# Performance work log

Measured on AMD Instinct MI355X. Metric: run time of the kernel, lower is better.

Reference implementation:

```python
import jax, jax.numpy as jnp
import numpy as np

N = 2_000_000  # total nodes across batch
F = 16         # eigenvector coefficient dim
B = 8          # number of graphs in batch (2^B sign combos)

def setup_inputs() -> dict:
    key = jax.random.key(0)
    k1, k2, k3 = jax.random.split(key, 3)
    inp = jax.random.normal(k1, (N, F), dtype=jnp.float32)
    tgt = jax.random.normal(k2, (N, F), dtype=jnp.float32)
    batch = jnp.sort(jax.random.randint(k3, (N,), 0, B, dtype=jnp.int32))
    return {"input": inp, "target": tgt, "batch": batch, "batch_size": B}

def reference(input, target, batch, batch_size):
    # loss(s) = sum((s_{batch} * x - t)^2) = sum(x^2) + sum(t^2) - 2 * sum_g s_g * dot_g
    # where dot_g = sum_{i in graph g} <x_i, t_i>.  Min over s in {+1,-1}^B is the
    # exact value produced by the original 2^B brute-force loop (reduction='sum').
    per_node = jnp.sum(input * target, axis=-1)                      # [N]
    dots = jax.ops.segment_sum(per_node, batch, num_segments=batch_size)  # [B]
    base = jnp.sum(input * input) + jnp.sum(target * target)         # scalar
    # enumerate all 2^B sign combinations (tiny, graph-level)
    idx = jnp.arange(2 ** batch_size)
    bits = (idx[:, None] >> jnp.arange(batch_size)[None, :]) & 1     # [2^B, B]
    signs = (1 - 2 * bits).astype(dots.dtype)                        # {+1,-1}
    losses = base - 2.0 * (signs @ dots)                             # [2^B]
    return jnp.min(losses)
```

## Files before the change

### kernel.cpp

```cpp
#include <hip/hip_runtime.h>

#define BLOCK 256
#define GRID  2048
#define NGRAPH 8
#define U 4
#define TILE (BLOCK * U)


__global__ __launch_bounds__(BLOCK) void reduce_kernel(
    const float4* __restrict__ x4,
    const float4* __restrict__ t4,
    const int*    __restrict__ batch,
    float* __restrict__ g_acc,
    int M )
{
    __shared__ float s_acc[NGRAPH + 1];
    const int tid = threadIdx.x;
    if (tid < NGRAPH + 1) s_acc[tid] = 0.0f;
    __syncthreads();

    float acc[NGRAPH];
    #pragma unroll
    for (int i = 0; i < NGRAPH; ++i) acc[i] = 0.0f;
    float base = 0.0f;

    const int nfull  = M / TILE;
    const int ntiles = (M + TILE - 1) / TILE;

    #define ACCUM(a, c, b)                                                 \
        do {                                                               \
            base += a.x*a.x + a.y*a.y + a.z*a.z + a.w*a.w                  \
                  + c.x*c.x + c.y*c.y + c.z*c.z + c.w*c.w;                 \
            const float d_ = a.x*c.x + a.y*c.y + a.z*c.z + a.w*c.w;        \
            _Pragma("unroll")                                              \
            for (int i = 0; i < NGRAPH; ++i)                               \
                acc[i] += (b == i) ? d_ : 0.0f;                            \
        } while (0)

    for (int t = blockIdx.x; t < ntiles; t += GRID) {
        const int e0 = t * TILE + tid;
        if (t < nfull) {
            const float4 a0 = x4[e0            ];
            const float4 a1 = x4[e0 +     BLOCK];
            const float4 a2 = x4[e0 + 2 * BLOCK];
            const float4 a3 = x4[e0 + 3 * BLOCK];
            const float4 c0 = t4[e0            ];
            const float4 c1 = t4[e0 +     BLOCK];
            const float4 c2 = t4[e0 + 2 * BLOCK];
            const float4 c3 = t4[e0 + 3 * BLOCK];
            const int    b0 = batch[(e0            ) >> 2];
            const int    b1 = batch[(e0 +     BLOCK) >> 2];
            const int    b2 = batch[(e0 + 2 * BLOCK) >> 2];
            const int    b3 = batch[(e0 + 3 * BLOCK) >> 2];

            ACCUM(a0, c0, b0);
            ACCUM(a1, c1, b1);
            ACCUM(a2, c2, b2);
            ACCUM(a3, c3, b3);
        } else {
            #pragma unroll
            for (int j = 0; j < U; ++j) {
                const int e = e0 + j * BLOCK;
                if (e < M) {
                    const float4 a = x4[e];
                    const float4 c = t4[e];
                    const int    b = batch[e >> 2];
                    ACCUM(a, c, b);
                }
            }
        }
    }
    #undef ACCUM

    #pragma unroll
    for (int i = 0; i <= NGRAPH; ++i) {
        float v = (i < NGRAPH) ? acc[i] : base;
        #pragma unroll
        for (int off = 32; off > 0; off >>= 1)
            v += __shfl_xor(v, off, 64);
        if ((tid & 63) == 0)
            atomicAdd(&s_acc[i], v);
    }
    __syncthreads();

    if (tid <= NGRAPH)
        atomicAdd(&g_acc[tid], s_acc[tid]);
}

__global__ void finalize_kernel(const float* __restrict__ g_acc,
                                float* __restrict__ out)
{
    if (threadIdx.x == 0) {
        float s = 0.0f;
        #pragma unroll
        for (int i = 0; i < NGRAPH; ++i) s += fabsf(g_acc[i]);
        out[0] = g_acc[NGRAPH] - 2.0f * s;
    }
}

extern "C" void kernel_launch(void* const* d_in, const int* in_sizes, int n_in,
                              void* d_out, int out_size, void* d_ws, size_t ws_size,
                              hipStream_t stream) {
    const float* inp   = (const float*)d_in[0];
    const float* tgt   = (const float*)d_in[1];
    const int*   batch = (const int*)d_in[2];

    const long long Nrows = (long long)in_sizes[0] / 16;
    const int       M     = (int)(Nrows * 4);

    float* g_acc = (float*)d_ws;
    hipMemsetAsync(g_acc, 0, (NGRAPH + 1) * sizeof(float), stream);

    reduce_kernel<<<GRID, BLOCK, 0, stream>>>(
        (const float4*)inp, (const float4*)tgt, batch, g_acc, M);

    finalize_kernel<<<1, 64, 0, stream>>>(g_acc, (float*)d_out);
}
```

Before: 276.3 us.

## Software-pipeline tile loads with double-buffered registers and sched barriers

Reorganizes the grid-stride loop into a two-stage software pipeline: the next tile's loads are issued into a second register set before the current tile is consumed, and sched_barrier calls stop the compiler from reordering them. The per-tile unroll drops from 4 to 2 so the two buffers keep register use similar, and the partial tail tile is handled once after the loop. The goal is to keep more memory requests in flight per wave on this bandwidth-bound reduction. In exchange, each tile carries fewer loads, and the fixed scheduling may block optimizations the compiler would otherwise make.

```diff
diff --git a/kernel.cpp b/kernel.cpp
--- a/kernel.cpp
+++ b/kernel.cpp
@@ -3,7 +3,7 @@
 #define BLOCK 256
 #define GRID  2048
 #define NGRAPH 8
-#define U 4
+#define U 2
 #define TILE (BLOCK * U)
 
 
@@ -24,8 +24,10 @@
     for (int i = 0; i < NGRAPH; ++i) acc[i] = 0.0f;
     float base = 0.0f;
 
+    const int bx     = blockIdx.x;
     const int nfull  = M / TILE;
     const int ntiles = (M + TILE - 1) / TILE;
+    const int k = (bx < nfull) ? ((nfull - 1 - bx) / GRID + 1) : 0;
 
     #define ACCUM(a, c, b)                                                 \
         do {                                                               \
@@ -37,40 +39,61 @@
                 acc[i] += (b == i) ? d_ : 0.0f;                            \
         } while (0)
 
-    for (int t = blockIdx.x; t < ntiles; t += GRID) {
-        const int e0 = t * TILE + tid;
-        if (t < nfull) {
-            const float4 a0 = x4[e0            ];
-            const float4 a1 = x4[e0 +     BLOCK];
-            const float4 a2 = x4[e0 + 2 * BLOCK];
-            const float4 a3 = x4[e0 + 3 * BLOCK];
-            const float4 c0 = t4[e0            ];
-            const float4 c1 = t4[e0 +     BLOCK];
-            const float4 c2 = t4[e0 + 2 * BLOCK];
-            const float4 c3 = t4[e0 + 3 * BLOCK];
-            const int    b0 = batch[(e0            ) >> 2];
-            const int    b1 = batch[(e0 +     BLOCK) >> 2];
-            const int    b2 = batch[(e0 + 2 * BLOCK) >> 2];
-            const int    b3 = batch[(e0 + 3 * BLOCK) >> 2];
+    float4 Aa0, Aa1, Ac0, Ac1;  int Ab0, Ab1;
+    float4 Ba0, Ba1, Bc0, Bc1;  int Bb0, Bb1;
 
-            ACCUM(a0, c0, b0);
-            ACCUM(a1, c1, b1);
-            ACCUM(a2, c2, b2);
-            ACCUM(a3, c3, b3);
+    #define LOAD_A(t)                                                      \
+        do { const int e_ = (t) * TILE + tid;                              \
+             Aa0 = x4[e_]; Aa1 = x4[e_ + BLOCK];                           \
+             Ac0 = t4[e_]; Ac1 = t4[e_ + BLOCK];                           \
+             Ab0 = batch[e_ >> 2]; Ab1 = batch[(e_ + BLOCK) >> 2]; } while (0)
+    #define LOAD_B(t)                                                      \
+        do { const int e_ = (t) * TILE + tid;                              \
+             Ba0 = x4[e_]; Ba1 = x4[e_ + BLOCK];                           \
+             Bc0 = t4[e_]; Bc1 = t4[e_ + BLOCK];                           \
+             Bb0 = batch[e_ >> 2]; Bb1 = batch[(e_ + BLOCK) >> 2]; } while (0)
+    #define CONS_A() do { ACCUM(Aa0, Ac0, Ab0); ACCUM(Aa1, Ac1, Ab1); } while (0)
+    #define CONS_B() do { ACCUM(Ba0, Bc0, Bb0); ACCUM(Ba1, Bc1, Bb1); } while (0)
+
+    if (k > 0) {
+        LOAD_A(bx);
+        int i = 1;
+        for (; i + 1 < k; i += 2) {
+            LOAD_B(bx + i * GRID);
+            __builtin_amdgcn_sched_barrier(0);
+            CONS_A();
+            LOAD_A(bx + (i + 1) * GRID);
+            __builtin_amdgcn_sched_barrier(0);
+            CONS_B();
+        }
+        if (i < k) {
+            LOAD_B(bx + i * GRID);
+            __builtin_amdgcn_sched_barrier(0);
+            CONS_A();
+            CONS_B();
         } else {
-            #pragma unroll
-            for (int j = 0; j < U; ++j) {
-                const int e = e0 + j * BLOCK;
-                if (e < M) {
-                    const float4 a = x4[e];
-                    const float4 c = t4[e];
-                    const int    b = batch[e >> 2];
-                    ACCUM(a, c, b);
-                }
+            CONS_A();
+        }
+    }
+
+    if (ntiles > nfull && (nfull % GRID) == bx) {
+        const int e0 = nfull * TILE + tid;
+        #pragma unroll
+        for (int j = 0; j < U; ++j) {
+            const int e = e0 + j * BLOCK;
+            if (e < M) {
+                const float4 a = x4[e];
+                const float4 c = t4[e];
+                const int    b = batch[e >> 2];
+                ACCUM(a, c, b);
             }
         }
     }
     #undef ACCUM
+    #undef LOAD_A
+    #undef LOAD_B
+    #undef CONS_A
+    #undef CONS_B
 
     #pragma unroll
     for (int i = 0; i <= NGRAPH; ++i) {
```

Result: no change. 276.0 us (-0.1%).
